# Kernel optimization log

Measured on AMD Instinct MI355X. Metric: run time of the kernel, lower is better.

The kernel has to match this reference:

```python
import jax, jax.numpy as jnp
import numpy as np

N_NODES = 50000
N_EDGES = 1600000
IN_DIM = 16
HID = 128
N_ITER = 3
EPS = 1e-8


def _rownorm(x):
    # x / (||x||_2 per row + 1e-8), matching torch.norm(p='fro', dim=1, keepdim=True)
    return x / (jnp.linalg.norm(x, axis=-1, keepdims=True) + EPS)


def setup_inputs() -> dict:
    key = jax.random.key(0)
    ks = jax.random.split(key, 16)
    s = 0.05  # small init scale for numerical sanity
    inp = {
        'feat': jax.random.normal(ks[0], (N_NODES, IN_DIM), dtype=jnp.float32),
        'src': jax.random.randint(ks[1], (N_EDGES,), 0, N_NODES, dtype=jnp.int32),
        'dst': jax.random.randint(ks[2], (N_EDGES,), 0, N_NODES, dtype=jnp.int32),
        'init_W0': jax.random.normal(ks[3], (IN_DIM, HID), dtype=jnp.float32) * s,
        'init_b0': jnp.zeros((HID,), dtype=jnp.float32),
        'init_W1': jax.random.normal(ks[4], (HID, HID), dtype=jnp.float32) * s,
        'init_b1': jnp.zeros((HID,), dtype=jnp.float32),
        'init_W2': jax.random.normal(ks[5], (HID, HID), dtype=jnp.float32) * s,
        'init_b2': jnp.zeros((HID,), dtype=jnp.float32),
        'node_W0': jax.random.normal(ks[6], (N_ITER, 3 * HID, HID), dtype=jnp.float32) * s,
        'node_b0': jnp.zeros((N_ITER, HID), dtype=jnp.float32),
        'node_W1': jax.random.normal(ks[7], (N_ITER, HID, HID), dtype=jnp.float32) * s,
        'node_b1': jnp.zeros((N_ITER, HID), dtype=jnp.float32),
        'node_W2': jax.random.normal(ks[8], (N_ITER, HID, HID), dtype=jnp.float32) * s,
        'node_b2': jnp.zeros((N_ITER, HID), dtype=jnp.float32),
    }
    return inp


def reference(feat, src, dst,
              init_W0, init_b0, init_W1, init_b1, init_W2, init_b2,
              node_W0, node_b0, node_W1, node_b1, node_W2, node_b2):
    n = feat.shape[0]

    # init_network: MLP (Linear+ReLU for hidden layers, linear output)
    h = jax.nn.relu(feat @ init_W0 + init_b0)
    h = jax.nn.relu(h @ init_W1 + init_b1)
    h = h @ init_W2 + init_b2  # [N, HID]

    # global representation: normalized sum over all nodes (single graph)
    gr = _rownorm(jnp.sum(h, axis=0, keepdims=True))  # [1, HID]

    # DGL update_all only updates nodes with >=1 incoming edge
    deg = jax.ops.segment_sum(jnp.ones_like(src, dtype=jnp.float32), dst,
                              num_segments=n)
    has_in = (deg > 0)[:, None]  # [N, 1]

    for i in range(node_W0.shape[0]):
        # copy_u + mailbox sum == gather src features, segment-sum by dst
        msg = jax.ops.segment_sum(h[src], dst, num_segments=n)  # [N, HID]
        inp = jnp.concatenate(
            [msg, h, jnp.broadcast_to(gr, (n, gr.shape[1]))], axis=1)  # [N, 3*HID]
        out = jax.nn.relu(inp @ node_W0[i] + node_b0[i])
        out = jax.nn.relu(out @ node_W1[i] + node_b1[i])
        out = out @ node_W2[i] + node_b2[i]
        out = _rownorm(out)
        h = jnp.where(has_in, out, h)
        gr = _rownorm(jnp.sum(h, axis=0, keepdims=True))

    return h
```

## Files before the change

kernel.cpp:

```cpp
#include <hip/hip_runtime.h>
#include <hip/hip_bf16.h>

#define HID 128
#define IN_DIM 16
#define LDST 136
#define NBSH 6
#define BPAD 16
#define SRCM 0x3ffffffu
#define CH 8192
#define NBMAX 1024
#define NDPW 4

typedef unsigned short u16;
typedef __attribute__((ext_vector_type(8))) short short8;
typedef __attribute__((ext_vector_type(4))) float f32x4;

__device__ __forceinline__ u16 f2b(float f) {
    unsigned u = __float_as_uint(f);
    return (u16)((u + 0x7FFF + ((u >> 16) & 1)) >> 16);
}


__global__ __launch_bounds__(1024) void bscan_k(const int* __restrict__ bktcnt, int* __restrict__ bktbase,
                                                int* __restrict__ bcnt, int* __restrict__ row_ptr,
                                                int nb, int n, int E) {
    __shared__ int sbuf[1024];
    int t = threadIdx.x;
    int v = (t < nb) ? bktcnt[t] : 0;
    sbuf[t] = v;
    __syncthreads();
    for (int off = 1; off < 1024; off <<= 1) {
        int a = (t >= off) ? sbuf[t - off] : 0;
        __syncthreads();
        sbuf[t] += a;
        __syncthreads();
    }
    if (t < nb) {
        int excl = sbuf[t] - v;
        bktbase[t] = excl;
        bcnt[t * BPAD] = excl;
    }
    if (t == 0) { bktbase[nb] = E; row_ptr[n] = E; }
}

__global__ __launch_bounds__(256) void bin_k(const int* __restrict__ src, const int* __restrict__ dst,
                                             int* __restrict__ bcnt, unsigned* __restrict__ ebuf,
                                             int E, int nb) {
    __shared__ unsigned stage[CH];
    __shared__ u16 sbk[CH];
    __shared__ int hist[NBMAX];
    __shared__ int lofs[NBMAX];
    __shared__ int sbase[NBMAX];
    __shared__ int scan256[256];
    int tid = threadIdx.x;
    int base = blockIdx.x * CH;
    int cnt = E - base; if (cnt > CH) cnt = CH;

    for (int i = tid; i < nb; i += 256) hist[i] = 0;
    __syncthreads();
    for (int j = tid; j < cnt; j += 256) {
        int d = dst[base + j];
        atomicAdd(&hist[d >> NBSH], 1);
    }
    __syncthreads();
    int psum[4];
    int ts = 0;
#pragma unroll
    for (int q = 0; q < 4; q++) {
        int idx = tid * 4 + q;
        int hv = (idx < nb) ? hist[idx] : 0;
        psum[q] = ts;
        ts += hv;
    }
    scan256[tid] = ts;
    __syncthreads();
    for (int off = 1; off < 256; off <<= 1) {
        int a = (tid >= off) ? scan256[tid - off] : 0;
        __syncthreads();
        scan256[tid] += a;
        __syncthreads();
    }
    int tbase = (tid > 0) ? scan256[tid - 1] : 0;
#pragma unroll
    for (int q = 0; q < 4; q++) {
        int idx = tid * 4 + q;
        if (idx < nb) lofs[idx] = tbase + psum[q];
    }
    __syncthreads();
    for (int i = tid; i < nb; i += 256) {
        int c = hist[i];
        if (c > 0) {
            int g = atomicAdd(&bcnt[i * BPAD], c);
            sbase[i] = g - lofs[i];
        }
    }
    __syncthreads();
    for (int j = tid; j < cnt; j += 256) {
        int e = base + j;
        int d = dst[e];
        int b = d >> NBSH;
        int r = atomicAdd(&lofs[b], 1);
        stage[r] = (unsigned)src[e] | ((unsigned)(d & 63) << 26);
        sbk[r] = (u16)b;
    }
    __syncthreads();
    for (int s = tid; s < cnt; s += 256) {
        int b = sbk[s];
        ebuf[sbase[b] + s] = stage[s];
    }
}


struct WJobs {
    const float* src[16];
    int dstoff[16];
    int ks[16];
};

__global__ __launch_bounds__(256) void preph_k(WJobs j, u16* __restrict__ Wt,
                                               const int* __restrict__ dst, int* __restrict__ bktcnt,
                                               float* __restrict__ gsums, int gz,
                                               int E, int nb, int nj) {
    __shared__ int hist[NBMAX];
    int tid = threadIdx.x;
    if ((int)blockIdx.x >= nj) {
        int base = (blockIdx.x - nj) * CH;
        int cnt = E - base; if (cnt > CH) cnt = CH;
        for (int i = tid; i < nb; i += 256) hist[i] = 0;
        __syncthreads();
        for (int jx = tid; jx < cnt; jx += 256) atomicAdd(&hist[dst[base + jx] >> NBSH], 1);
        __syncthreads();
        for (int i = tid; i < nb; i += 256) {
            int c = hist[i];
            if (c > 0) atomicAdd(&bktcnt[i], c);
        }
        return;
    }
    int m = blockIdx.x;
    if (m == 0) {
        for (int i = tid; i < gz; i += 256) gsums[i] = 0.f;
    }
    const float* s = j.src[m];
    u16* d = Wt + j.dstoff[m];
    if (j.ks[m] == 5) {
        for (int idx = tid; idx < 4096; idx += 256) {
            int jj = idx & 7;
            int lane = (idx >> 3) & 63;
            int ni = (idx >> 9) & 3;
            int half = (idx >> 11) & 1;
            int k = ((lane >> 4) << 3) + jj;
            int col = half * 64 + ni * 16 + (lane & 15);
            d[idx] = (k < IN_DIM) ? f2b(s[k * HID + col]) : (u16)0;
        }
    } else {
        for (int idx = tid; idx < 16384; idx += 256) {
            int jj = idx & 7;
            int lane = (idx >> 3) & 63;
            int ni = (idx >> 9) & 3;
            int kk = (idx >> 11) & 3;
            int half = idx >> 13;
            int k = kk * 32 + (lane >> 4) * 8 + jj;
            int col = half * 64 + ni * 16 + (lane & 15);
            d[idx] = f2b(s[k * HID + col]);
        }
    }
}



__device__ __forceinline__ void unpack_add(uint4 v, float* a) {
    a[0] += __uint_as_float(v.x << 16);
    a[1] += __uint_as_float(v.x & 0xffff0000u);
    a[2] += __uint_as_float(v.y << 16);
    a[3] += __uint_as_float(v.y & 0xffff0000u);
    a[4] += __uint_as_float(v.z << 16);
    a[5] += __uint_as_float(v.z & 0xffff0000u);
    a[6] += __uint_as_float(v.w << 16);
    a[7] += __uint_as_float(v.w & 0xffff0000u);
}

__global__ __launch_bounds__(256) void msg_k(const u16* __restrict__ hb, const int* __restrict__ row_ptr,
                                             const int* __restrict__ srcs, u16* __restrict__ msgb, int n,
                                             const float* __restrict__ gsumIn, const float* __restrict__ Wg,
                                             const float* __restrict__ b0, float* __restrict__ grW) {
    if (blockIdx.x == gridDim.x - 1) {
        __shared__ float sred[2];
        __shared__ float sgr[HID];
        int t = threadIdx.x;
        if (t < HID) {
            float g = gsumIn[t];
            float s = g * g;
#pragma unroll
            for (int off = 1; off < 64; off <<= 1) s += __shfl_xor(s, off);
            if ((t & 63) == 0) sred[t >> 6] = s;
        }
        __syncthreads();
        if (t < HID) {
            float inv = 1.f / (sqrtf(sred[0] + sred[1]) + 1e-8f);
            sgr[t] = gsumIn[t] * inv;
        }
        __syncthreads();
        if (t < HID) {
            float a = b0[t];
#pragma unroll 4
            for (int k = 0; k < HID; k++) a += sgr[k] * Wg[k * HID + t];
            grW[t] = a;
        }
        return;
    }
    int wave = threadIdx.x >> 6, lane = threadIdx.x & 63;
    int g = lane >> 4;
    int l16 = lane & 15;
    int d0 = (blockIdx.x * 4 + wave) * NDPW;
    if (d0 >= n) return;
    int eNext = row_ptr[d0];
#pragma unroll 1
    for (int k = 0; k < NDPW; k++) {
        int d = d0 + k;
        if (d >= n) break;
        int e = eNext;
        int e1 = row_ptr[d + 1];
        eNext = e1;
        float a[8] = {0.f, 0.f, 0.f, 0.f, 0.f, 0.f, 0.f, 0.f};
        int s0 = 0, s1 = 0, s2 = 0, s3 = 0;
        if (e + 15 < e1) {
            s0 = srcs[e + g]; s1 = srcs[e + 4 + g];
            s2 = srcs[e + 8 + g]; s3 = srcs[e + 12 + g];
        }
        while (e + 15 < e1) {
            int t0 = s0, t1 = s1, t2 = s2, t3 = s3;
            int en = e + 16;
            if (en + 15 < e1) {
                s0 = srcs[en + g]; s1 = srcs[en + 4 + g];
                s2 = srcs[en + 8 + g]; s3 = srcs[en + 12 + g];
            }
            uint4 v0 = *(const uint4*)(hb + (size_t)t0 * HID + l16 * 8);
            uint4 v1 = *(const uint4*)(hb + (size_t)t1 * HID + l16 * 8);
            uint4 v2 = *(const uint4*)(hb + (size_t)t2 * HID + l16 * 8);
            uint4 v3 = *(const uint4*)(hb + (size_t)t3 * HID + l16 * 8);
            unpack_add(v0, a);
            unpack_add(v1, a);
            unpack_add(v2, a);
            unpack_add(v3, a);
            e = en;
        }
        if (e + 7 < e1) {
            int t0 = srcs[e + g], t1 = srcs[e + 4 + g];
            uint4 v0 = *(const uint4*)(hb + (size_t)t0 * HID + l16 * 8);
            uint4 v1 = *(const uint4*)(hb + (size_t)t1 * HID + l16 * 8);
            unpack_add(v0, a);
            unpack_add(v1, a);
            e += 8;
        }
        if (e + 3 < e1) {
            int s = srcs[e + g];
            uint4 v = *(const uint4*)(hb + (size_t)s * HID + l16 * 8);
            unpack_add(v, a);
            e += 4;
        }
        if (e + g < e1) {
            int s = srcs[e + g];
            uint4 v = *(const uint4*)(hb + (size_t)s * HID + l16 * 8);
            unpack_add(v, a);
        }
#pragma unroll
        for (int i = 0; i < 8; i++) {
            a[i] += __shfl_xor(a[i], 16);
            a[i] += __shfl_xor(a[i], 32);
        }
        if (g == 0) {
            uint4 o;
            o.x = (unsigned)f2b(a[0]) | ((unsigned)f2b(a[1]) << 16);
            o.y = (unsigned)f2b(a[2]) | ((unsigned)f2b(a[3]) << 16);
            o.z = (unsigned)f2b(a[4]) | ((unsigned)f2b(a[5]) << 16);
            o.w = (unsigned)f2b(a[6]) | ((unsigned)f2b(a[7]) << 16);
            *(uint4*)(msgb + (size_t)d * HID + l16 * 8) = o;
        }
    }
}


__device__ __forceinline__ void load_tile64(const u16* __restrict__ base, int tid, uint4 p[4]) {
#pragma unroll
    for (int q = 0; q < 4; q++) {
        int c = tid + q * 256;
        p[q] = *(const uint4*)(base + (size_t)(c >> 4) * HID + (c & 15) * 8);
    }
}

__device__ __forceinline__ void write_tile64(const uint4 p[4], int tid, u16* s) {
#pragma unroll
    for (int q = 0; q < 4; q++) {
        int c = tid + q * 256;
        *(uint4*)(s + (c >> 4) * LDST + (c & 15) * 8) = p[q];
    }
}

__device__ __forceinline__ void macF(const u16* sA, const u16* __restrict__ Wf, int wrow, int half,
                                     int lane, int ln15, int quad, f32x4 acc[2][4]) {
    const u16* wb = Wf + (size_t)half * 8192;
#pragma unroll
    for (int kk = 0; kk < 4; kk++) {
        short8 a[2], b[4];
#pragma unroll
        for (int mi = 0; mi < 2; mi++)
            a[mi] = *(const short8*)(sA + (wrow + mi * 16 + ln15) * LDST + kk * 32 + quad * 8);
#pragma unroll
        for (int ni = 0; ni < 4; ni++)
            b[ni] = *(const short8*)(wb + (size_t)(((kk * 4 + ni) * 64) + lane) * 8);
#pragma unroll
        for (int mi = 0; mi < 2; mi++)
#pragma unroll
            for (int ni = 0; ni < 4; ni++)
                acc[mi][ni] = __builtin_amdgcn_mfma_f32_16x16x32_bf16(a[mi], b[ni], acc[mi][ni], 0, 0, 0);
    }
}

__device__ __forceinline__ void set_bias(f32x4 acc[2][4], const float* bias, int wcol, int ln15) {
#pragma unroll
    for (int ni = 0; ni < 4; ni++) {
        float bv = bias[wcol + ni * 16 + ln15];
#pragma unroll
        for (int mi = 0; mi < 2; mi++) acc[mi][ni] = (f32x4){bv, bv, bv, bv};
    }
}

__device__ __forceinline__ void acc_to_sA(const f32x4 acc[2][4], u16* sA, int wrow, int wcol,
                                          int ln15, int quad) {
#pragma unroll
    for (int mi = 0; mi < 2; mi++)
#pragma unroll
        for (int r = 0; r < 4; r++) {
            int row = wrow + mi * 16 + quad * 4 + r;
#pragma unroll
            for (int ni = 0; ni < 4; ni++)
                sA[row * LDST + wcol + ni * 16 + ln15] = f2b(fmaxf(acc[mi][ni][r], 0.f));
        }
}


__global__ __launch_bounds__(256) void f2init_k(const unsigned* __restrict__ ebuf, const int* __restrict__ bktbase,
                                                int* __restrict__ row_ptr, int* __restrict__ deg,
                                                int* __restrict__ srcs,
                                                const float* __restrict__ feat,
                                                const u16* __restrict__ W0f, const u16* __restrict__ W1f,
                                                const u16* __restrict__ W2f,
                                                const float* __restrict__ b0, const float* __restrict__ b1,
                                                const float* __restrict__ b2,
                                                float* __restrict__ h, u16* __restrict__ hb,
                                                float* __restrict__ gsum0, int n, int nbk) {
    __shared__ u16 s0[64 * LDST];
    __shared__ u16 s1[64 * LDST];
    int tid = threadIdx.x;
    if ((int)blockIdx.x < nbk) {
        int* hist64 = (int*)s0;
        int* lofs = (int*)s0 + 64;
        int b = blockIdx.x;
        int e0 = bktbase[b], e1 = bktbase[b + 1];
        if (tid < 64) hist64[tid] = 0;
        __syncthreads();
        for (int i = e0 + tid; i < e1; i += 256) atomicAdd(&hist64[ebuf[i] >> 26], 1);
        __syncthreads();
        if (tid < 64) {
            int d = hist64[tid];
            int s = d;
#pragma unroll
            for (int off = 1; off < 64; off <<= 1) {
                int t = __shfl_up(s, off);
                if (tid >= off) s += t;
            }
            int excl = e0 + s - d;
            int gi = (b << NBSH) + tid;
            if (gi < n) { row_ptr[gi] = excl; deg[gi] = d; }
            lofs[tid] = excl;
        }
        __syncthreads();
        for (int i = e0 + tid; i < e1; i += 256) {
            unsigned p = ebuf[i];
            int d = (int)(p >> 26);
            int pos = atomicAdd(&lofs[d], 1);
            srcs[pos] = (int)(p & SRCM);
        }
        return;
    }
    int lane = tid & 63, wave = tid >> 6;
    int ln15 = lane & 15, quad = lane >> 4;
    int wrow = (wave >> 1) * 32, half = wave & 1, wcol = half * 64;
    int row0 = (blockIdx.x - nbk) * 64;
    f32x4 acc[2][4];

    {
        int row = tid >> 2, coff = tid & 3;
        ushort4 o = make_ushort4(0, 0, 0, 0);
        if (row0 + row < n) {
            float4 v = *(const float4*)(feat + (size_t)(row0 + row) * IN_DIM + coff * 4);
            o = make_ushort4(f2b(v.x), f2b(v.y), f2b(v.z), f2b(v.w));
        }
        *(ushort4*)(s0 + row * LDST + coff * 4) = o;
        *(ushort4*)(s0 + row * LDST + 16 + coff * 4) = make_ushort4(0, 0, 0, 0);
    }
    set_bias(acc, b0, wcol, ln15);
    __syncthreads();
    {
        short8 a[2], b[4];
#pragma unroll
        for (int mi = 0; mi < 2; mi++)
            a[mi] = *(const short8*)(s0 + (wrow + mi * 16 + ln15) * LDST + quad * 8);
#pragma unroll
        for (int ni = 0; ni < 4; ni++)
            b[ni] = *(const short8*)(W0f + (size_t)((half * 4 + ni) * 64 + lane) * 8);
#pragma unroll
        for (int mi = 0; mi < 2; mi++)
#pragma unroll
            for (int ni = 0; ni < 4; ni++)
                acc[mi][ni] = __builtin_amdgcn_mfma_f32_16x16x32_bf16(a[mi], b[ni], acc[mi][ni], 0, 0, 0);
    }
    acc_to_sA(acc, s1, wrow, wcol, ln15, quad);
    set_bias(acc, b1, wcol, ln15);
    __syncthreads();
    macF(s1, W1f, wrow, half, lane, ln15, quad, acc);
    acc_to_sA(acc, s0, wrow, wcol, ln15, quad);
    set_bias(acc, b2, wcol, ln15);
    __syncthreads();
    macF(s0, W2f, wrow, half, lane, ln15, quad, acc);

    float csum[4] = {0.f, 0.f, 0.f, 0.f};
#pragma unroll
    for (int mi = 0; mi < 2; mi++)
#pragma unroll
        for (int r = 0; r < 4; r++) {
            int row = row0 + wrow + mi * 16 + quad * 4 + r;
            if (row < n) {
#pragma unroll
                for (int ni = 0; ni < 4; ni++) {
                    float v = acc[mi][ni][r];
                    int col = wcol + ni * 16 + ln15;
                    h[(size_t)row * HID + col] = v;
                    hb[(size_t)row * HID + col] = f2b(v);
                    csum[ni] += v;
                }
            }
        }
    __syncthreads();
    float* s_cs = (float*)s1;
    if (tid < HID) s_cs[tid] = 0.f;
    __syncthreads();
#pragma unroll
    for (int ni = 0; ni < 4; ni++) {
        float p = csum[ni];
        p += __shfl_xor(p, 16);
        p += __shfl_xor(p, 32);
        if (quad == 0) atomicAdd(&s_cs[wcol + ni * 16 + ln15], p);
    }
    __syncthreads();
    if (tid < HID) atomicAdd(&gsum0[tid], s_cs[tid]);
}


template <bool FINAL>
__global__ __launch_bounds__(256, 4) void node_fused_k(const u16* __restrict__ msgb, const u16* __restrict__ hbin,
                                                       const u16* __restrict__ W0af, const u16* __restrict__ W0bf,
                                                       const u16* __restrict__ W1f, const u16* __restrict__ W2f,
                                                       const float* __restrict__ grW,
                                                       const float* __restrict__ b1, const float* __restrict__ b2,
                                                       const int* __restrict__ deg,
                                                       float* __restrict__ h, u16* __restrict__ hb,
                                                       float* __restrict__ gsumOut, int n) {
    __shared__ u16 s0[64 * LDST];
    __shared__ u16 s1[64 * LDST];
    int tid = threadIdx.x;
    int lane = tid & 63, wave = tid >> 6;
    int ln15 = lane & 15, quad = lane >> 4;
    int wrow = (wave >> 1) * 32, half = wave & 1, wcol = half * 64;
    int row0 = blockIdx.x * 64;
    f32x4 acc[2][4];

    {
        uint4 tM[4], tH[4];
        load_tile64(msgb + (size_t)row0 * HID, tid, tM);
        load_tile64(hbin + (size_t)row0 * HID, tid, tH);
        write_tile64(tM, tid, s0);
        write_tile64(tH, tid, s1);
    }
    set_bias(acc, grW, wcol, ln15);
    __syncthreads();
    macF(s0, W0af, wrow, half, lane, ln15, quad, acc);
    macF(s1, W0bf, wrow, half, lane, ln15, quad, acc);
    __syncthreads();
    acc_to_sA(acc, s0, wrow, wcol, ln15, quad);
    set_bias(acc, b1, wcol, ln15);
    __syncthreads();
    macF(s0, W1f, wrow, half, lane, ln15, quad, acc);
    acc_to_sA(acc, s1, wrow, wcol, ln15, quad);
    set_bias(acc, b2, wcol, ln15);
    __syncthreads();
    macF(s1, W2f, wrow, half, lane, ln15, quad, acc);

    __syncthreads();
    float* s_rs = (float*)s0;
    float* s_cs = (float*)s0 + 64;
    if (tid < 64) s_rs[tid] = 0.f;
    else if (tid < 192) s_cs[tid - 64] = 0.f;
    __syncthreads();
#pragma unroll
    for (int mi = 0; mi < 2; mi++)
#pragma unroll
        for (int r = 0; r < 4; r++) {
            float p = 0.f;
#pragma unroll
            for (int ni = 0; ni < 4; ni++) { float v = acc[mi][ni][r]; p += v * v; }
            p += __shfl_xor(p, 1); p += __shfl_xor(p, 2);
            p += __shfl_xor(p, 4); p += __shfl_xor(p, 8);
            if (ln15 == 0) atomicAdd(&s_rs[wrow + mi * 16 + quad * 4 + r], p);
        }
    __syncthreads();
    float csum[4] = {0.f, 0.f, 0.f, 0.f};
#pragma unroll
    for (int mi = 0; mi < 2; mi++)
#pragma unroll
        for (int r = 0; r < 4; r++) {
            int rl = wrow + mi * 16 + quad * 4 + r;
            int row = row0 + rl;
            if (row < n) {
                bool upd = deg[row] > 0;
                float inv = 1.f / (sqrtf(s_rs[rl]) + 1e-8f);
#pragma unroll
                for (int ni = 0; ni < 4; ni++) {
                    int col = wcol + ni * 16 + ln15;
                    if (FINAL) {
                        if (upd) h[(size_t)row * HID + col] = acc[mi][ni][r] * inv;
                    } else {
                        float v;
                        if (upd) {
                            v = acc[mi][ni][r] * inv;
                            hb[(size_t)row * HID + col] = f2b(v);
                        } else {
                            v = h[(size_t)row * HID + col];
                        }
                        csum[ni] += v;
                    }
                }
            }
        }
    if (!FINAL) {
#pragma unroll
        for (int ni = 0; ni < 4; ni++) {
            float p = csum[ni];
            p += __shfl_xor(p, 16);
            p += __shfl_xor(p, 32);
            if (quad == 0) atomicAdd(&s_cs[wcol + ni * 16 + ln15], p);
        }
        __syncthreads();
        if (tid < HID) atomicAdd(&gsumOut[tid], s_cs[tid]);
    }
}


static inline char* align_up(char* p, size_t a) {
    return (char*)(((uintptr_t)p + a - 1) & ~(uintptr_t)(a - 1));
}

extern "C" void kernel_launch(void* const* d_in, const int* in_sizes, int n_in,
                              void* d_out, int out_size, void* d_ws, size_t ws_size,
                              hipStream_t stream) {
    const float* feat = (const float*)d_in[0];
    const int* src = (const int*)d_in[1];
    const int* dst = (const int*)d_in[2];
    const float* iW0 = (const float*)d_in[3];
    const float* ib0 = (const float*)d_in[4];
    const float* iW1 = (const float*)d_in[5];
    const float* ib1 = (const float*)d_in[6];
    const float* iW2 = (const float*)d_in[7];
    const float* ib2 = (const float*)d_in[8];
    const float* nW0 = (const float*)d_in[9];
    const float* nb0 = (const float*)d_in[10];
    const float* nW1 = (const float*)d_in[11];
    const float* nb1 = (const float*)d_in[12];
    const float* nW2 = (const float*)d_in[13];
    const float* nb2 = (const float*)d_in[14];

    int N = in_sizes[0] / IN_DIM;
    int E = in_sizes[1];
    int n_iter = in_sizes[10] / HID;
    int NB = (N + (1 << NBSH) - 1) >> NBSH;
    float* h = (float*)d_out;

    char* w = (char*)d_ws;
    size_t big2 = (size_t)(N + 128) * HID * sizeof(u16);
    u16* hb   = (u16*)w; w += big2;
    u16* msgb = (u16*)w; w += big2;
    float* gsums = (float*)w; w += (size_t)(n_iter + 1) * HID * sizeof(float);
    float* grW = (float*)w; w += 1024;
    u16* Wt = (u16*)w; w += (size_t)(4096 + 2 * 16384 + n_iter * 4 * 16384) * sizeof(u16);
    w = align_up(w, 16);
    int* deg = (int*)w; w += (size_t)N * 4;  w = align_up(w, 16);
    int* row_ptr = (int*)w; w += (size_t)(N + 1) * 4;  w = align_up(w, 16);
    int* bktcnt = (int*)w; w += (size_t)NB * 4;  w = align_up(w, 16);
    int* bktbase = (int*)w; w += (size_t)(NB + 1) * 4;  w = align_up(w, 64);
    int* bcnt = (int*)w; w += (size_t)NB * BPAD * 4;  w = align_up(w, 16);
    int* srcs = (int*)w; w += (size_t)E * 4;  w = align_up(w, 16);
    unsigned* ebuf = (unsigned*)w; w += (size_t)E * 4;
    (void)ws_size; (void)n_in; (void)out_size;

    const int OFF_IW0 = 0;
    const int OFF_IW1 = 4096;
    const int OFF_IW2 = 4096 + 16384;
    const int OFF_IT = 4096 + 2 * 16384;

    WJobs jobs;
    int nj = 0;
    jobs.src[nj] = iW0; jobs.dstoff[nj] = OFF_IW0; jobs.ks[nj] = 5; nj++;
    jobs.src[nj] = iW1; jobs.dstoff[nj] = OFF_IW1; jobs.ks[nj] = 8; nj++;
    jobs.src[nj] = iW2; jobs.dstoff[nj] = OFF_IW2; jobs.ks[nj] = 8; nj++;
    for (int i = 0; i < n_iter && nj + 4 <= 16; i++) {
        int base = OFF_IT + i * 4 * 16384;
        jobs.src[nj] = nW0 + (size_t)i * 3 * HID * HID;               jobs.dstoff[nj] = base;             jobs.ks[nj] = 8; nj++;
        jobs.src[nj] = nW0 + (size_t)i * 3 * HID * HID + HID * HID;   jobs.dstoff[nj] = base + 16384;     jobs.ks[nj] = 8; nj++;
        jobs.src[nj] = nW1 + (size_t)i * HID * HID;                   jobs.dstoff[nj] = base + 2 * 16384; jobs.ks[nj] = 8; nj++;
        jobs.src[nj] = nW2 + (size_t)i * HID * HID;                   jobs.dstoff[nj] = base + 3 * 16384; jobs.ks[nj] = 8; nj++;
    }

    hipMemsetAsync(bktcnt, 0, (size_t)NB * 4, stream);

    int cg = (E + CH - 1) / CH;
    preph_k<<<nj + cg, 256, 0, stream>>>(jobs, Wt, dst, bktcnt,
                                         gsums, (n_iter + 1) * HID, E, NB, nj);
    bscan_k<<<1, 1024, 0, stream>>>(bktcnt, bktbase, bcnt, row_ptr, NB, N, E);
    bin_k<<<cg, 256, 0, stream>>>(src, dst, bcnt, ebuf, E, NB);

    int gbi = (N + 63) / 64;
    f2init_k<<<NB + gbi, 256, 0, stream>>>(ebuf, bktbase, row_ptr, deg, srcs,
                                           feat, Wt + OFF_IW0, Wt + OFF_IW1, Wt + OFF_IW2,
                                           ib0, ib1, ib2, h, hb, gsums, N, NB);

    int gb2 = (N + 63) / 64;
    int dpb = 4 * NDPW;
    int rb = (N + dpb - 1) / dpb;
    for (int i = 0; i < n_iter; i++) {
        const u16* Wit = Wt + OFF_IT + (size_t)i * 4 * 16384;
        const float* Wg = nW0 + (size_t)i * 3 * HID * HID + 2 * HID * HID;
        msg_k<<<rb + 1, 256, 0, stream>>>(hb, row_ptr, srcs, msgb, N,
                                          gsums + (size_t)i * HID, Wg, nb0 + (size_t)i * HID, grW);
        if (i + 1 < n_iter) {
            node_fused_k<false><<<gb2, 256, 0, stream>>>(msgb, hb, Wit, Wit + 16384, Wit + 2 * 16384,
                                                         Wit + 3 * 16384, grW, nb1 + (size_t)i * HID,
                                                         nb2 + (size_t)i * HID, deg, h, hb,
                                                         gsums + (size_t)(i + 1) * HID, N);
        } else {
            node_fused_k<true><<<gb2, 256, 0, stream>>>(msgb, hb, Wit, Wit + 16384, Wit + 2 * 16384,
                                                        Wit + 3 * 16384, grW, nb1 + (size_t)i * HID,
                                                        nb2 + (size_t)i * HID, deg, h, hb,
                                                        nullptr, N);
        }
    }
}
```

Before: 425.5 us.

## Fuse message aggregation into node MLP kernel with ping-pong bf16 buffers

```diff
diff --git a/kernel.cpp b/kernel.cpp
--- a/kernel.cpp
+++ b/kernel.cpp
@@ -9,7 +9,6 @@
 #define SRCM 0x3ffffffu
 #define CH 8192
 #define NBMAX 1024
-#define NDPW 4
 
 typedef unsigned short u16;
 typedef __attribute__((ext_vector_type(8))) short short8;
@@ -167,7 +166,6 @@
 }
 
 
-
 __device__ __forceinline__ void unpack_add(uint4 v, float* a) {
     a[0] += __uint_as_float(v.x << 16);
     a[1] += __uint_as_float(v.x & 0xffff0000u);
@@ -179,107 +177,6 @@
     a[7] += __uint_as_float(v.w & 0xffff0000u);
 }
 
-__global__ __launch_bounds__(256) void msg_k(const u16* __restrict__ hb, const int* __restrict__ row_ptr,
-                                             const int* __restrict__ srcs, u16* __restrict__ msgb, int n,
-                                             const float* __restrict__ gsumIn, const float* __restrict__ Wg,
-                                             const float* __restrict__ b0, float* __restrict__ grW) {
-    if (blockIdx.x == gridDim.x - 1) {
-        __shared__ float sred[2];
-        __shared__ float sgr[HID];
-        int t = threadIdx.x;
-        if (t < HID) {
-            float g = gsumIn[t];
-            float s = g * g;
-#pragma unroll
-            for (int off = 1; off < 64; off <<= 1) s += __shfl_xor(s, off);
-            if ((t & 63) == 0) sred[t >> 6] = s;
-        }
-        __syncthreads();
-        if (t < HID) {
-            float inv = 1.f / (sqrtf(sred[0] + sred[1]) + 1e-8f);
-            sgr[t] = gsumIn[t] * inv;
-        }
-        __syncthreads();
-        if (t < HID) {
-            float a = b0[t];
-#pragma unroll 4
-            for (int k = 0; k < HID; k++) a += sgr[k] * Wg[k * HID + t];
-            grW[t] = a;
-        }
-        return;
-    }
-    int wave = threadIdx.x >> 6, lane = threadIdx.x & 63;
-    int g = lane >> 4;
-    int l16 = lane & 15;
-    int d0 = (blockIdx.x * 4 + wave) * NDPW;
-    if (d0 >= n) return;
-    int eNext = row_ptr[d0];
-#pragma unroll 1
-    for (int k = 0; k < NDPW; k++) {
-        int d = d0 + k;
-        if (d >= n) break;
-        int e = eNext;
-        int e1 = row_ptr[d + 1];
-        eNext = e1;
-        float a[8] = {0.f, 0.f, 0.f, 0.f, 0.f, 0.f, 0.f, 0.f};
-        int s0 = 0, s1 = 0, s2 = 0, s3 = 0;
-        if (e + 15 < e1) {
-            s0 = srcs[e + g]; s1 = srcs[e + 4 + g];
-            s2 = srcs[e + 8 + g]; s3 = srcs[e + 12 + g];
-        }
-        while (e + 15 < e1) {
-            int t0 = s0, t1 = s1, t2 = s2, t3 = s3;
-            int en = e + 16;
-            if (en + 15 < e1) {
-                s0 = srcs[en + g]; s1 = srcs[en + 4 + g];
-                s2 = srcs[en + 8 + g]; s3 = srcs[en + 12 + g];
-            }
-            uint4 v0 = *(const uint4*)(hb + (size_t)t0 * HID + l16 * 8);
-            uint4 v1 = *(const uint4*)(hb + (size_t)t1 * HID + l16 * 8);
-            uint4 v2 = *(const uint4*)(hb + (size_t)t2 * HID + l16 * 8);
-            uint4 v3 = *(const uint4*)(hb + (size_t)t3 * HID + l16 * 8);
-            unpack_add(v0, a);
-            unpack_add(v1, a);
-            unpack_add(v2, a);
-            unpack_add(v3, a);
-            e = en;
-        }
-        if (e + 7 < e1) {
-            int t0 = srcs[e + g], t1 = srcs[e + 4 + g];
-            uint4 v0 = *(const uint4*)(hb + (size_t)t0 * HID + l16 * 8);
-            uint4 v1 = *(const uint4*)(hb + (size_t)t1 * HID + l16 * 8);
-            unpack_add(v0, a);
-            unpack_add(v1, a);
-            e += 8;
-        }
-        if (e + 3 < e1) {
-            int s = srcs[e + g];
-            uint4 v = *(const uint4*)(hb + (size_t)s * HID + l16 * 8);
-            unpack_add(v, a);
-            e += 4;
-        }
-        if (e + g < e1) {
-            int s = srcs[e + g];
-            uint4 v = *(const uint4*)(hb + (size_t)s * HID + l16 * 8);
-            unpack_add(v, a);
-        }
-#pragma unroll
-        for (int i = 0; i < 8; i++) {
-            a[i] += __shfl_xor(a[i], 16);
-            a[i] += __shfl_xor(a[i], 32);
-        }
-        if (g == 0) {
-            uint4 o;
-            o.x = (unsigned)f2b(a[0]) | ((unsigned)f2b(a[1]) << 16);
-            o.y = (unsigned)f2b(a[2]) | ((unsigned)f2b(a[3]) << 16);
-            o.z = (unsigned)f2b(a[4]) | ((unsigned)f2b(a[5]) << 16);
-            o.w = (unsigned)f2b(a[6]) | ((unsigned)f2b(a[7]) << 16);
-            *(uint4*)(msgb + (size_t)d * HID + l16 * 8) = o;
-        }
-    }
-}
-
-
 __device__ __forceinline__ void load_tile64(const u16* __restrict__ base, int tid, uint4 p[4]) {
 #pragma unroll
     for (int q = 0; q < 4; q++) {
@@ -336,6 +233,29 @@
             for (int ni = 0; ni < 4; ni++)
                 sA[row * LDST + wcol + ni * 16 + ln15] = f2b(fmaxf(acc[mi][ni][r], 0.f));
         }
+}
+
+__device__ __forceinline__ void macF16(const u16* s, const u16* __restrict__ Wf, int wrow4, int half,
+                                       int nib, int lane, int ln15, int quad, f32x4 acc[2]) {
+    const u16* wb = Wf + (size_t)half * 8192;
+#pragma unroll
+    for (int kk = 0; kk < 4; kk++) {
+        short8 a = *(const short8*)(s + (wrow4 + ln15) * LDST + kk * 32 + quad * 8);
+#pragma unroll
+        for (int j = 0; j < 2; j++) {
+            short8 b = *(const short8*)(wb + (size_t)(((kk * 4 + nib + j) * 64) + lane) * 8);
+            acc[j] = __builtin_amdgcn_mfma_f32_16x16x32_bf16(a, b, acc[j], 0, 0, 0);
+        }
+    }
+}
+
+__device__ __forceinline__ void acc_to16(const f32x4 acc[2], u16* s, int wrow4, int wcol,
+                                         int ln15, int quad) {
+#pragma unroll
+    for (int j = 0; j < 2; j++)
+#pragma unroll
+        for (int r = 0; r < 4; r++)
+            s[(wrow4 + quad * 4 + r) * LDST + wcol + j * 16 + ln15] = f2b(fmaxf(acc[j][r], 0.f));
 }
 
 
@@ -458,97 +378,200 @@
 
 
 template <bool FINAL>
-__global__ __launch_bounds__(256, 4) void node_fused_k(const u16* __restrict__ msgb, const u16* __restrict__ hbin,
-                                                       const u16* __restrict__ W0af, const u16* __restrict__ W0bf,
-                                                       const u16* __restrict__ W1f, const u16* __restrict__ W2f,
-                                                       const float* __restrict__ grW,
-                                                       const float* __restrict__ b1, const float* __restrict__ b2,
-                                                       const int* __restrict__ deg,
-                                                       float* __restrict__ h, u16* __restrict__ hb,
-                                                       float* __restrict__ gsumOut, int n) {
+__global__ __launch_bounds__(1024, 8) void node_merged_k(const u16* __restrict__ hbR, u16* __restrict__ hbW,
+                                                         const int* __restrict__ row_ptr, const int* __restrict__ srcs,
+                                                         const u16* __restrict__ W0af, const u16* __restrict__ W0bf,
+                                                         const u16* __restrict__ W1f, const u16* __restrict__ W2f,
+                                                         const float* __restrict__ gsumIn, const float* __restrict__ Wg,
+                                                         const float* __restrict__ b0v, const float* __restrict__ b1,
+                                                         const float* __restrict__ b2, const int* __restrict__ deg,
+                                                         float* __restrict__ h, float* __restrict__ gsumOut, int n) {
     __shared__ u16 s0[64 * LDST];
     __shared__ u16 s1[64 * LDST];
+    __shared__ float sgp[8][HID];
+    __shared__ float sgrw[HID];
+    __shared__ float sred[2];
     int tid = threadIdx.x;
     int lane = tid & 63, wave = tid >> 6;
     int ln15 = lane & 15, quad = lane >> 4;
-    int wrow = (wave >> 1) * 32, half = wave & 1, wcol = half * 64;
     int row0 = blockIdx.x * 64;
-    f32x4 acc[2][4];
-
+
+    if (tid < HID) {
+        float g = gsumIn[tid];
+        float s = g * g;
+#pragma unroll
+        for (int off = 1; off < 64; off <<= 1) s += __shfl_xor(s, off);
+        if ((tid & 63) == 0) sred[tid >> 6] = s;
+    }
     {
-        uint4 tM[4], tH[4];
-        load_tile64(msgb + (size_t)row0 * HID, tid, tM);
-        load_tile64(hbin + (size_t)row0 * HID, tid, tH);
-        write_tile64(tM, tid, s0);
-        write_tile64(tH, tid, s1);
-    }
-    set_bias(acc, grW, wcol, ln15);
-    __syncthreads();
-    macF(s0, W0af, wrow, half, lane, ln15, quad, acc);
-    macF(s1, W0bf, wrow, half, lane, ln15, quad, acc);
-    __syncthreads();
-    acc_to_sA(acc, s0, wrow, wcol, ln15, quad);
-    set_bias(acc, b1, wcol, ln15);
-    __syncthreads();
-    macF(s0, W1f, wrow, half, lane, ln15, quad, acc);
-    acc_to_sA(acc, s1, wrow, wcol, ln15, quad);
-    set_bias(acc, b2, wcol, ln15);
-    __syncthreads();
-    macF(s1, W2f, wrow, half, lane, ln15, quad, acc);
-
-    __syncthreads();
+        int row = tid >> 4, ch = tid & 15;
+        uint4 v = *(const uint4*)(hbR + (size_t)(row0 + row) * HID + ch * 8);
+        *(uint4*)(s1 + row * LDST + ch * 8) = v;
+    }
+    __syncthreads();
+    {
+        float inv = 1.f / (sqrtf(sred[0] + sred[1]) + 1e-8f);
+        int col = tid & 127, kq = tid >> 7;
+        float p = 0.f;
+#pragma unroll 4
+        for (int k2 = 0; k2 < 16; k2++) {
+            int k = kq * 16 + k2;
+            p += gsumIn[k] * Wg[(size_t)k * HID + col];
+        }
+        sgp[kq][col] = p;
+        __syncthreads();
+        if (tid < HID)
+            sgrw[tid] = b0v[tid] + inv * (sgp[0][tid] + sgp[1][tid] + sgp[2][tid] + sgp[3][tid] +
+                                          sgp[4][tid] + sgp[5][tid] + sgp[6][tid] + sgp[7][tid]);
+    }
+
+    {
+        int g = quad, l16 = ln15;
+        int d0 = row0 + wave * 4;
+        int eNext = (d0 < n) ? row_ptr[d0] : 0;
+#pragma unroll 1
+        for (int k = 0; k < 4; k++) {
+            int d = d0 + k;
+            int rl = wave * 4 + k;
+            if (d >= n) {
+                if (g == 0) *(uint4*)(s0 + (size_t)rl * LDST + l16 * 8) = make_uint4(0, 0, 0, 0);
+                continue;
+            }
+            int e = eNext;
+            int e1 = row_ptr[d + 1];
+            eNext = e1;
+            float a[8] = {0.f, 0.f, 0.f, 0.f, 0.f, 0.f, 0.f, 0.f};
+            int s0i = 0, s1i = 0, s2i = 0, s3i = 0;
+            if (e + 15 < e1) {
+                s0i = srcs[e + g]; s1i = srcs[e + 4 + g];
+                s2i = srcs[e + 8 + g]; s3i = srcs[e + 12 + g];
+            }
+            while (e + 15 < e1) {
+                int t0 = s0i, t1 = s1i, t2 = s2i, t3 = s3i;
+                int en = e + 16;
+                if (en + 15 < e1) {
+                    s0i = srcs[en + g]; s1i = srcs[en + 4 + g];
+                    s2i = srcs[en + 8 + g]; s3i = srcs[en + 12 + g];
+                }
+                uint4 v0 = *(const uint4*)(hbR + (size_t)t0 * HID + l16 * 8);
+                uint4 v1 = *(const uint4*)(hbR + (size_t)t1 * HID + l16 * 8);
+                uint4 v2 = *(const uint4*)(hbR + (size_t)t2 * HID + l16 * 8);
+                uint4 v3 = *(const uint4*)(hbR + (size_t)t3 * HID + l16 * 8);
+                unpack_add(v0, a);
+                unpack_add(v1, a);
+                unpack_add(v2, a);
+                unpack_add(v3, a);
+                e = en;
+            }
+            if (e + 7 < e1) {
+                int t0 = srcs[e + g], t1 = srcs[e + 4 + g];
+                uint4 v0 = *(const uint4*)(hbR + (size_t)t0 * HID + l16 * 8);
+                uint4 v1 = *(const uint4*)(hbR + (size_t)t1 * HID + l16 * 8);
+                unpack_add(v0, a);
+                unpack_add(v1, a);
+                e += 8;
+            }
+            if (e + 3 < e1) {
+                int s = srcs[e + g];
+                uint4 v = *(const uint4*)(hbR + (size_t)s * HID + l16 * 8);
+                unpack_add(v, a);
+                e += 4;
+            }
+            if (e + g < e1) {
+                int s = srcs[e + g];
+                uint4 v = *(const uint4*)(hbR + (size_t)s * HID + l16 * 8);
+                unpack_add(v, a);
+            }
+#pragma unroll
+            for (int i = 0; i < 8; i++) {
+                a[i] += __shfl_xor(a[i], 16);
+                a[i] += __shfl_xor(a[i], 32);
+            }
+            if (g == 0) {
+                uint4 o;
+                o.x = (unsigned)f2b(a[0]) | ((unsigned)f2b(a[1]) << 16);
+                o.y = (unsigned)f2b(a[2]) | ((unsigned)f2b(a[3]) << 16);
+                o.z = (unsigned)f2b(a[4]) | ((unsigned)f2b(a[5]) << 16);
+                o.w = (unsigned)f2b(a[6]) | ((unsigned)f2b(a[7]) << 16);
+                *(uint4*)(s0 + (size_t)rl * LDST + l16 * 8) = o;
+            }
+        }
+    }
+
+    int wrow4 = (wave & 3) * 16;
+    int wcol = (wave >> 2) * 32;
+    int half = wave >> 3;
+    int nib = ((wave >> 2) & 1) * 2;
+    f32x4 acc[2];
+    __syncthreads();
+#pragma unroll
+    for (int j = 0; j < 2; j++) {
+        float bv = sgrw[wcol + j * 16 + ln15];
+        acc[j] = (f32x4){bv, bv, bv, bv};
+    }
+    macF16(s0, W0af, wrow4, half, nib, lane, ln15, quad, acc);
+    macF16(s1, W0bf, wrow4, half, nib, lane, ln15, quad, acc);
+    __syncthreads();
+    acc_to16(acc, s0, wrow4, wcol, ln15, quad);
+#pragma unroll
+    for (int j = 0; j < 2; j++) {
+        float bv = b1[wcol + j * 16 + ln15];
+        acc[j] = (f32x4){bv, bv, bv, bv};
+    }
+    __syncthreads();
+    macF16(s0, W1f, wrow4, half, nib, lane, ln15, quad, acc);
+    acc_to16(acc, s1, wrow4, wcol, ln15, quad);
+#pragma unroll
+    for (int j = 0; j < 2; j++) {
+        float bv = b2[wcol + j * 16 + ln15];
+        acc[j] = (f32x4){bv, bv, bv, bv};
+    }
+    __syncthreads();
+    macF16(s1, W2f, wrow4, half, nib, lane, ln15, quad, acc);
+
     float* s_rs = (float*)s0;
     float* s_cs = (float*)s0 + 64;
     if (tid < 64) s_rs[tid] = 0.f;
     else if (tid < 192) s_cs[tid - 64] = 0.f;
     __syncthreads();
 #pragma unroll
-    for (int mi = 0; mi < 2; mi++)
-#pragma unroll
-        for (int r = 0; r < 4; r++) {
-            float p = 0.f;
-#pragma unroll
-            for (int ni = 0; ni < 4; ni++) { float v = acc[mi][ni][r]; p += v * v; }
-            p += __shfl_xor(p, 1); p += __shfl_xor(p, 2);
-            p += __shfl_xor(p, 4); p += __shfl_xor(p, 8);
-            if (ln15 == 0) atomicAdd(&s_rs[wrow + mi * 16 + quad * 4 + r], p);
-        }
-    __syncthreads();
-    float csum[4] = {0.f, 0.f, 0.f, 0.f};
-#pragma unroll
-    for (int mi = 0; mi < 2; mi++)
-#pragma unroll
-        for (int r = 0; r < 4; r++) {
-            int rl = wrow + mi * 16 + quad * 4 + r;
-            int row = row0 + rl;
-            if (row < n) {
-                bool upd = deg[row] > 0;
-                float inv = 1.f / (sqrtf(s_rs[rl]) + 1e-8f);
-#pragma unroll
-                for (int ni = 0; ni < 4; ni++) {
-                    int col = wcol + ni * 16 + ln15;
-                    if (FINAL) {
-                        if (upd) h[(size_t)row * HID + col] = acc[mi][ni][r] * inv;
-                    } else {
-                        float v;
-                        if (upd) {
-                            v = acc[mi][ni][r] * inv;
-                            hb[(size_t)row * HID + col] = f2b(v);
-                        } else {
-                            v = h[(size_t)row * HID + col];
-                        }
-                        csum[ni] += v;
-                    }
+    for (int r = 0; r < 4; r++) {
+        float p = acc[0][r] * acc[0][r] + acc[1][r] * acc[1][r];
+        p += __shfl_xor(p, 1); p += __shfl_xor(p, 2);
+        p += __shfl_xor(p, 4); p += __shfl_xor(p, 8);
+        if (ln15 == 0) atomicAdd(&s_rs[wrow4 + quad * 4 + r], p);
+    }
+    __syncthreads();
+    float csum[2] = {0.f, 0.f};
+#pragma unroll
+    for (int r = 0; r < 4; r++) {
+        int rl = wrow4 + quad * 4 + r;
+        int row = row0 + rl;
+        if (row < n) {
+            bool upd = deg[row] > 0;
+            float inv2 = 1.f / (sqrtf(s_rs[rl]) + 1e-8f);
+#pragma unroll
+            for (int j = 0; j < 2; j++) {
+                int col = wcol + j * 16 + ln15;
+                if (FINAL) {
+                    if (upd) h[(size_t)row * HID + col] = acc[j][r] * inv2;
+                } else {
+                    float v;
+                    if (upd) v = acc[j][r] * inv2;
+                    else v = h[(size_t)row * HID + col];
+                    hbW[(size_t)row * HID + col] = f2b(v);
+                    csum[j] += v;
                 }
             }
         }
+    }
     if (!FINAL) {
 #pragma unroll
-        for (int ni = 0; ni < 4; ni++) {
-            float p = csum[ni];
+        for (int j = 0; j < 2; j++) {
+            float p = csum[j];
             p += __shfl_xor(p, 16);
             p += __shfl_xor(p, 32);
-            if (quad == 0) atomicAdd(&s_cs[wcol + ni * 16 + ln15], p);
+            if (quad == 0) atomicAdd(&s_cs[wcol + j * 16 + ln15], p);
         }
         __syncthreads();
         if (tid < HID) atomicAdd(&gsumOut[tid], s_cs[tid]);
@@ -587,8 +610,8 @@
 
     char* w = (char*)d_ws;
     size_t big2 = (size_t)(N + 128) * HID * sizeof(u16);
-    u16* hb   = (u16*)w; w += big2;
-    u16* msgb = (u16*)w; w += big2;
+    u16* hb0  = (u16*)w; w += big2;
+    u16* hb1  = (u16*)w; w += big2;
     float* gsums = (float*)w; w += (size_t)(n_iter + 1) * HID * sizeof(float);
     float* grW = (float*)w; w += 1024;
     u16* Wt = (u16*)w; w += (size_t)(4096 + 2 * 16384 + n_iter * 4 * 16384) * sizeof(u16);
@@ -600,7 +623,7 @@
     int* bcnt = (int*)w; w += (size_t)NB * BPAD * 4;  w = align_up(w, 16);
     int* srcs = (int*)w; w += (size_t)E * 4;  w = align_up(w, 16);
     unsigned* ebuf = (unsigned*)w; w += (size_t)E * 4;
-    (void)ws_size; (void)n_in; (void)out_size;
+    (void)ws_size; (void)n_in; (void)out_size; (void)grW;
 
     const int OFF_IW0 = 0;
     const int OFF_IW1 = 4096;
@@ -631,26 +654,27 @@
     int gbi = (N + 63) / 64;
     f2init_k<<<NB + gbi, 256, 0, stream>>>(ebuf, bktbase, row_ptr, deg, srcs,
                                            feat, Wt + OFF_IW0, Wt + OFF_IW1, Wt + OFF_IW2,
-                                           ib0, ib1, ib2, h, hb, gsums, N, NB);
+                                           ib0, ib1, ib2, h, hb0, gsums, N, NB);
 
     int gb2 = (N + 63) / 64;
-    int dpb = 4 * NDPW;
-    int rb = (N + dpb - 1) / dpb;
+    const u16* cur = hb0;
+    u16* nxt = hb1;
     for (int i = 0; i < n_iter; i++) {
         const u16* Wit = Wt + OFF_IT + (size_t)i * 4 * 16384;
         const float* Wg = nW0 + (size_t)i * 3 * HID * HID + 2 * HID * HID;
-        msg_k<<<rb + 1, 256, 0, stream>>>(hb, row_ptr, srcs, msgb, N,
-                                          gsums + (size_t)i * HID, Wg, nb0 + (size_t)i * HID, grW);
         if (i + 1 < n_iter) {
-            node_fused_k<false><<<gb2, 256, 0, stream>>>(msgb, hb, Wit, Wit + 16384, Wit + 2 * 16384,
-                                                         Wit + 3 * 16384, grW, nb1 + (size_t)i * HID,
-                                                         nb2 + (size_t)i * HID, deg, h, hb,
-                                                         gsums + (size_t)(i + 1) * HID, N);
+            node_merged_k<false><<<gb2, 1024, 0, stream>>>(cur, nxt, row_ptr, srcs,
+                                                           Wit, Wit + 16384, Wit + 2 * 16384, Wit + 3 * 16384,
+                                                           gsums + (size_t)i * HID, Wg, nb0 + (size_t)i * HID,
+                                                           nb1 + (size_t)i * HID, nb2 + (size_t)i * HID, deg,
+                                                           h, gsums + (size_t)(i + 1) * HID, N);
         } else {
-            node_fused_k<true><<<gb2, 256, 0, stream>>>(msgb, hb, Wit, Wit + 16384, Wit + 2 * 16384,
-                                                        Wit + 3 * 16384, grW, nb1 + (size_t)i * HID,
-                                                        nb2 + (size_t)i * HID, deg, h, hb,
-                                                        nullptr, N);
-        }
-    }
-}
+            node_merged_k<true><<<gb2, 1024, 0, stream>>>(cur, nxt, row_ptr, srcs,
+                                                          Wit, Wit + 16384, Wit + 2 * 16384, Wit + 3 * 16384,
+                                                          gsums + (size_t)i * HID, Wg, nb0 + (size_t)i * HID,
+                                                          nb1 + (size_t)i * HID, nb2 + (size_t)i * HID, deg,
+                                                          h, nullptr, N);
+        }
+        u16* t = (u16*)cur; cur = nxt; nxt = t;
+    }
+}
```

Measured after the change: 467.8 us. +9.9%, slower.
